# Kernel tuning notes

Hardware: AMD Instinct MI355X
Metric: run time of the kernel (lower is better)

Reference implementation:

```python
import jax, jax.numpy as jnp
import numpy as np

NUM_HEAD = 8
HEAD_DIM = 64
LMK = 32          # num_landmarks
WIN = 128         # window_size
DIM = 512         # transformer_dim == num_head*head_dim
EXT = WIN // 2    # ext_len in get_tiles_v2
TILE = 2 * EXT + WIN  # 256
SCALE = 1.0 / np.sqrt(HEAD_DIM)
NEG_INF = float('-inf')


def layernorm(x, g, b, eps=1e-5):
    m = jnp.mean(x, axis=-1, keepdims=True)
    v = jnp.mean((x - m) ** 2, axis=-1, keepdims=True)
    return (x - m) * jax.lax.rsqrt(v + eps) * g + b


def split_heads(x):
    b, s, _ = x.shape
    return x.reshape(b, s, NUM_HEAD, HEAD_DIM).transpose(0, 2, 1, 3)


def setup_inputs() -> dict:
    key = jax.random.key(0)
    ks = jax.random.split(key, 8)
    B, S = 2, 8192
    w = lambda k, sh: (jax.random.normal(k, sh, jnp.float32) * 0.02)
    return {
        'X': jax.random.normal(ks[0], (B, S, DIM), jnp.float32),
        'mask': jnp.ones((B, S), jnp.bool_),
        'Wq_w': w(ks[1], (DIM, DIM)), 'Wq_b': jnp.zeros((DIM,), jnp.float32),
        'Wk_w': w(ks[2], (DIM, DIM)), 'Wk_b': jnp.zeros((DIM,), jnp.float32),
        'Wv_w': w(ks[3], (DIM, DIM)), 'Wv_b': jnp.zeros((DIM,), jnp.float32),
        'Wo_w': w(ks[4], (DIM, DIM)), 'Wo_b': jnp.zeros((DIM,), jnp.float32),
        'ln_l_g': jnp.ones((DIM,), jnp.float32), 'ln_l_b': jnp.zeros((DIM,), jnp.float32),
        'ln_s_g': jnp.ones((DIM,), jnp.float32), 'ln_s_b': jnp.zeros((DIM,), jnp.float32),
        'dconv_w': w(ks[5], (DIM, NUM_HEAD * LMK)), 'dconv_b': jnp.zeros((NUM_HEAD * LMK,), jnp.float32),
    }


def reference(X, mask, Wq_w, Wq_b, Wk_w, Wk_b, Wv_w, Wv_b, Wo_w, Wo_b,
              ln_l_g, ln_l_b, ln_s_g, ln_s_b, dconv_w, dconv_b):
    B, S, D = X.shape
    G = S // WIN  # number of window groups
    pad_mask = ~mask  # True where padded

    Q = split_heads(X @ Wq_w + Wq_b) * SCALE                       # [B,H,S,dh]
    K = split_heads(layernorm(X @ Wk_w + Wk_b, ln_l_g, ln_l_b))    # [B,H,S,dh]
    V = split_heads(layernorm(X @ Wv_w + Wv_b, ln_l_g, ln_l_b))    # [B,H,S,dh]

    # --- landmark (long-range) compression ---
    hs = X @ dconv_w + dconv_b                                     # [B,S,H*L]
    hs = jnp.where(pad_mask[:, :, None], NEG_INF, hs)
    hs = jax.nn.softmax(hs.astype(jnp.float32), axis=1).astype(X.dtype)
    hs = hs.reshape(B, S, NUM_HEAD, LMK).transpose(0, 2, 3, 1)     # [B,H,L,S]
    K_c = jnp.einsum('bhls,bhsd->bhld', hs, K)                     # [B,H,L,dh]
    V_c = jnp.einsum('bhls,bhsd->bhld', hs, V)
    # dual LayerNorm on compressed keys/values (over combined head dim)
    K_c = split_heads(layernorm(K_c.transpose(0, 2, 1, 3).reshape(B, LMK, D), ln_s_g, ln_s_b))
    V_c = split_heads(layernorm(V_c.transpose(0, 2, 1, 3).reshape(B, LMK, D), ln_s_g, ln_s_b))

    attn_compress = jnp.einsum('bhsd,bhld->bhsl', Q, K_c)          # [B,H,S,L]

    # --- sliding-window (short-range) scores, v2 tiling ---
    idx = jnp.arange(G)[:, None] * WIN + jnp.arange(TILE)[None, :]  # [G,TILE] indices into padded seq
    K_pad = jnp.pad(K, ((0, 0), (0, 0), (EXT, EXT), (0, 0)))
    K_tiles = K_pad[:, :, idx, :]                                   # [B,H,G,TILE,dh]
    mask_pad = jnp.pad(pad_mask, ((0, 0), (EXT, EXT)), constant_values=True)
    mask_tiles = mask_pad[:, idx]                                   # [B,G,TILE]
    Q_tiles = Q.reshape(B, NUM_HEAD, G, WIN, HEAD_DIM)
    win = jnp.einsum('bhgwd,bhgtd->bhgwt', Q_tiles, K_tiles)
    win = jnp.where(mask_tiles[:, None, :, None, :], NEG_INF, win)
    win = win.reshape(B, NUM_HEAD, S, TILE)

    # --- joint softmax over [landmarks | window] ---
    all_scores = jnp.concatenate([attn_compress, win], axis=-1)     # [B,H,S,L+TILE]
    probs = jax.nn.softmax(all_scores.astype(jnp.float32), axis=-1).astype(X.dtype)
    probs = jnp.where(pad_mask[:, None, :, None], 0.0, probs)

    C = jnp.einsum('bhsl,bhld->bhsd', probs[..., :LMK], V_c)        # landmark contribution
    win_p = probs[..., LMK:].reshape(B, NUM_HEAD, G, WIN, TILE)
    V_pad = jnp.pad(V, ((0, 0), (0, 0), (EXT, EXT), (0, 0)))
    V_tiles = V_pad[:, :, idx, :]                                   # [B,H,G,TILE,dh]
    C = C + jnp.einsum('bhgwt,bhgtd->bhgwd', win_p, V_tiles).reshape(B, NUM_HEAD, S, HEAD_DIM)

    out = C.transpose(0, 2, 1, 3).reshape(B, S, D) @ Wo_w + Wo_b
    return out
```

## Files before the change

kernel.cpp:

```cpp
#include <hip/hip_runtime.h>

typedef unsigned short u16;
typedef unsigned int u32;
typedef __attribute__((ext_vector_type(8))) short bf16x8;
typedef __attribute__((ext_vector_type(4))) float f32x4;

#define DEVI static __device__ __forceinline__

DEVI float bf2f(u16 u){ u32 x = ((u32)u) << 16; float f; __builtin_memcpy(&f, &x, 4); return f; }
DEVI u16 f2bf(float f){ u32 x; __builtin_memcpy(&x, &f, 4); u32 r = x + 0x7FFFu + ((x >> 16) & 1u); return (u16)(r >> 16); }
DEVI u32 pk2(float a, float b){ return ((u32)f2bf(b) << 16) | (u32)f2bf(a); }

DEVI f32x4 mfma16(bf16x8 a, bf16x8 b, f32x4 c){
  return __builtin_amdgcn_mfma_f32_16x16x32_bf16(a, b, c, 0, 0, 0);
}

typedef __attribute__((address_space(3))) u32* lds_ptr_t;
typedef const __attribute__((address_space(1))) u32* gbl_ptr_t;
DEVI void gload16(const void* g, const void* l){
  __builtin_amdgcn_global_load_lds((gbl_ptr_t)(unsigned long long)g,
                                   (lds_ptr_t)(unsigned long long)l,
                                   16, 0, 0);
}

__global__ void cvt_x_kernel(const float* __restrict__ X, u16* __restrict__ Xb){
  int i = blockIdx.x * 256 + threadIdx.x;
  const f32x4* p = (const f32x4*)X;
  f32x4 a = p[(size_t)i*2], c = p[(size_t)i*2 + 1];
  bf16x8 v;
  v[0]=(short)f2bf(a[0]); v[1]=(short)f2bf(a[1]); v[2]=(short)f2bf(a[2]); v[3]=(short)f2bf(a[3]);
  v[4]=(short)f2bf(c[0]); v[5]=(short)f2bf(c[1]); v[6]=(short)f2bf(c[2]); v[7]=(short)f2bf(c[3]);
  *(bf16x8*)(Xb + (size_t)i*8) = v;
}

__global__ void transpose_all(const float* __restrict__ Wq, const float* __restrict__ Wk,
                              const float* __restrict__ Wv, const float* __restrict__ Wd,
                              const float* __restrict__ Wo,
                              const float* __restrict__ Wqb, const float* __restrict__ Wkb,
                              const float* __restrict__ Wvb, const float* __restrict__ Wdb,
                              u16* __restrict__ WT, float* __restrict__ biasAll)
{
  int id = blockIdx.x;
  if (id >= 1152){
    int c = (id - 1152) * 256 + threadIdx.x;
    float v = (c < 512) ? Wqb[c] : (c < 1024) ? Wkb[c-512] : (c < 1536) ? Wvb[c-1024] : Wdb[c-1536];
    biasAll[c] = v;
    return;
  }
  const float* W; int RO, N, local;
  if      (id < 256){ W = Wq; RO = 0;    N = 512; local = id; }
  else if (id < 512){ W = Wk; RO = 512;  N = 512; local = id - 256; }
  else if (id < 768){ W = Wv; RO = 1024; N = 512; local = id - 512; }
  else if (id < 896){ W = Wd; RO = 1536; N = 256; local = id - 768; }
  else              { W = Wo; RO = 1792; N = 512; local = id - 896; }
  int ntiles = N >> 5;
  int n0 = (local & (ntiles - 1)) * 32, k0 = (local / ntiles) * 32;
  __shared__ float tile[32][33];
  int tx = threadIdx.x & 31, ty = threadIdx.x >> 5;
  #pragma unroll
  for (int i = 0; i < 32; i += 8)
    tile[ty + i][tx] = W[(size_t)(k0 + ty + i) * N + n0 + tx];
  __syncthreads();
  #pragma unroll
  for (int i = 0; i < 32; i += 8)
    WT[(size_t)(RO + n0 + ty + i) * 512 + k0 + tx] = f2bf(tile[tx][ty + i]);
}

template<int MODE>
__global__ __launch_bounds__(256, 2) void gemmP(
    const u16* __restrict__ Abase, const u16* __restrict__ WT, const float* __restrict__ biasAll,
    u16* __restrict__ Qb, u16* __restrict__ Kb, u16* __restrict__ Vb,
    float* __restrict__ hsf, float* __restrict__ cmx, float* __restrict__ csm,
    float* __restrict__ pstatV, float* __restrict__ Cf)
{
  __shared__ __align__(16) u16 smem[32768];
  const int t = threadIdx.x, lane = t & 63, w = t >> 6;
  const int wm = w >> 1, wn = w & 1;
  const int lrow = lane & 15, lk = lane >> 4;
  int by, bx;
  {
    int xcd = blockIdx.x & 7, c = blockIdx.x >> 3;
    if (MODE == 0){ by = xcd*16 + c/14;   bx = c % 14; }
    else          { by = xcd*16 + (c>>2); bx = c & 3; }
  }
  const int m0 = by*128, n0 = bx*128;
  const u16* Bb = (MODE == 0) ? WT : (WT + (size_t)1792*512);

  const int srow = w*32 + (lane >> 3);
  const int scol = ((lane & 7) ^ (lane >> 3)) * 8;
  const u16* sA = Abase + (size_t)(m0 + srow)*512 + scol;
  const u16* sB = Bb    + (size_t)(n0 + srow)*512 + scol;

  f32x4 acc[4][4];
  const f32x4 fz = {0.f,0.f,0.f,0.f};
  #pragma unroll
  for (int i = 0; i < 4; i++)
    #pragma unroll
    for (int j = 0; j < 4; j++) acc[i][j] = fz;

  auto stage = [&](int tt){
    int slot = tt & 1;
    #pragma unroll
    for (int i = 0; i < 4; i++){
      gload16(sA + tt*64 + (size_t)i*4096, smem + slot*8192 + (w*4 + i)*512);
      gload16(sB + tt*64 + (size_t)i*4096, smem + 16384 + slot*8192 + (w*4 + i)*512);
    }
  };

  stage(0);
  stage(1);

  const int swz = (lrow & 7);
  #pragma unroll
  for (int tt = 0; tt < 8; tt++){
    if (tt < 7) asm volatile("s_waitcnt vmcnt(8)" ::: "memory");
    else        asm volatile("s_waitcnt vmcnt(0)" ::: "memory");
    __builtin_amdgcn_s_barrier();
    const u16* aS = smem + (tt & 1)*8192;
    const u16* bS = smem + 16384 + (tt & 1)*8192;
    #pragma unroll
    for (int ks = 0; ks < 2; ks++){
      bf16x8 af[4], bfv[4];
      #pragma unroll
      for (int mi = 0; mi < 4; mi++){
        int r = wm*64 + mi*16 + lrow;
        af[mi] = *(const bf16x8*)(aS + (r*8 + ((ks*4 + lk) ^ swz))*8);
      }
      #pragma unroll
      for (int ni = 0; ni < 4; ni++){
        int r = wn*64 + ni*16 + lrow;
        bfv[ni] = *(const bf16x8*)(bS + (r*8 + ((ks*4 + lk) ^ swz))*8);
      }
      #pragma unroll
      for (int mi = 0; mi < 4; mi++)
        #pragma unroll
        for (int ni = 0; ni < 4; ni++)
          acc[mi][ni] = mfma16(bfv[ni], af[mi], acc[mi][ni]);
    }
    __builtin_amdgcn_s_barrier();
    if (tt + 2 < 8) stage(tt + 2);
  }

  if (MODE == 1){
    #pragma unroll
    for (int mi = 0; mi < 4; mi++){
      int grow = m0 + wm*64 + mi*16 + lrow;
      #pragma unroll
      for (int ni = 0; ni < 4; ni++){
        int gcol0 = n0 + wn*64 + ni*16 + lk*4;
        f32x4 bv4 = *(const f32x4*)(biasAll + gcol0);
        f32x4 vv;
        #pragma unroll
        for (int rr = 0; rr < 4; rr++) vv[rr] = acc[mi][ni][rr] + bv4[rr];
        *(f32x4*)(Cf + (size_t)grow*512 + gcol0) = vv;
      }
    }
    return;
  }

  if (bx < 12){
    const int sel = bx >> 2;
    u16* dst = (sel == 0) ? Qb : (sel == 1) ? Kb : Vb;
    const float scale = (sel == 0) ? 0.125f : 1.0f;
    f32x4 bv4s[4];
    #pragma unroll
    for (int ni = 0; ni < 4; ni++)
      bv4s[ni] = *(const f32x4*)(biasAll + n0 + wn*64 + ni*16 + lk*4);
    #pragma unroll
    for (int mi = 0; mi < 4; mi++){
      int grow = m0 + wm*64 + mi*16 + lrow;
      int b = grow >> 13, s = grow & 8191;
      #pragma unroll
      for (int ni = 0; ni < 4; ni++){
        int gcol0 = n0 + wn*64 + ni*16 + lk*4;
        int lcol0 = gcol0 & 511, hh = lcol0 >> 6, dd0 = lcol0 & 63;
        float v0 = (acc[mi][ni][0] + bv4s[ni][0]) * scale;
        float v1 = (acc[mi][ni][1] + bv4s[ni][1]) * scale;
        float v2 = (acc[mi][ni][2] + bv4s[ni][2]) * scale;
        float v3 = (acc[mi][ni][3] + bv4s[ni][3]) * scale;
        u32* p = (u32*)(dst + (((size_t)(b*8 + hh))*8192 + s)*64 + dd0);
        p[0] = pk2(v0, v1);
        p[1] = pk2(v2, v3);
      }
    }
    if (sel == 2){
      float* vst = (float*)smem;
      __syncthreads();
      #pragma unroll
      for (int mi = 0; mi < 4; mi++){
        float s = 0.f, q = 0.f;
        #pragma unroll
        for (int ni = 0; ni < 4; ni++)
          #pragma unroll
          for (int rr = 0; rr < 4; rr++){
            float v = acc[mi][ni][rr] + bv4s[ni][rr];
            s += v; q += v*v;
          }
        s += __shfl_xor(s, 16); q += __shfl_xor(q, 16);
        s += __shfl_xor(s, 32); q += __shfl_xor(q, 32);
        if (lk == 0){
          int rloc = wm*64 + mi*16 + lrow;
          vst[rloc*4 + wn*2]     = s;
          vst[rloc*4 + wn*2 + 1] = q;
        }
      }
      __syncthreads();
      if (t < 128){
        float s = vst[t*4+0] + vst[t*4+2];
        float q = vst[t*4+1] + vst[t*4+3];
        pstatV[(size_t)(m0 + t)*8 + (bx - 8)*2]     = s;
        pstatV[(size_t)(m0 + t)*8 + (bx - 8)*2 + 1] = q;
      }
    }
  } else {
    float* pm = (float*)smem;
    float* ps = pm + 256;
    __syncthreads();
    #pragma unroll
    for (int ni = 0; ni < 4; ni++){
      int gcol0 = n0 + wn*64 + ni*16 + lk*4;
      int c0 = gcol0 - 1536;
      f32x4 bv4 = *(const f32x4*)(biasAll + gcol0);
      float mx[4], sm[4];
      #pragma unroll
      for (int rr = 0; rr < 4; rr++){ mx[rr] = -1e30f; sm[rr] = 0.f; }
      #pragma unroll
      for (int mi = 0; mi < 4; mi++){
        int grow = m0 + wm*64 + mi*16 + lrow;
        f32x4 v;
        #pragma unroll
        for (int rr = 0; rr < 4; rr++){
          v[rr] = acc[mi][ni][rr] + bv4[rr];
          float nm = fmaxf(mx[rr], v[rr]);
          sm[rr] = sm[rr]*__expf(mx[rr] - nm) + __expf(v[rr] - nm);
          mx[rr] = nm;
        }
        *(f32x4*)(hsf + (size_t)grow*256 + c0) = v;
      }
      #pragma unroll
      for (int rr = 0; rr < 4; rr++){
        #pragma unroll
        for (int d2 = 1; d2 < 16; d2 <<= 1){
          float om = __shfl_xor(mx[rr], d2), os = __shfl_xor(sm[rr], d2);
          float nm = fmaxf(mx[rr], om);
          sm[rr] = sm[rr]*__expf(mx[rr] - nm) + os*__expf(om - nm);
          mx[rr] = nm;
        }
      }
      if (lrow == 0){
        int cl = wn*64 + ni*16 + lk*4;
        f32x4 m4 = {mx[0], mx[1], mx[2], mx[3]};
        f32x4 s4 = {sm[0], sm[1], sm[2], sm[3]};
        *(f32x4*)(pm + wm*128 + cl) = m4;
        *(f32x4*)(ps + wm*128 + cl) = s4;
      }
    }
    __syncthreads();
    if (t < 128){
      float ma = pm[t], mb = pm[128 + t];
      float nm = fmaxf(ma, mb);
      float s = ps[t]*__expf(ma - nm) + ps[128 + t]*__expf(mb - nm);
      int b = m0 >> 13, chunk = (m0 & 8191) >> 7;
      int c = (n0 - 1536) + t;
      cmx[((size_t)b*64 + chunk)*256 + c] = nm;
      csm[((size_t)b*64 + chunk)*256 + c] = s;
    }
  }
}

__global__ __launch_bounds__(256) void ln_k(u16* __restrict__ Kb,
    const float* __restrict__ gg, const float* __restrict__ bb)
{
  const int lane = threadIdx.x & 63, w = threadIdx.x >> 6;
  const int row = blockIdx.x * 4 + w;
  const int b = row >> 13, si = row & 8191;
  const int hh = lane >> 3, d = (lane & 7) * 8;
  u16* p = Kb + (((size_t)(b*8 + hh))*8192 + si)*64 + d;
  bf16x8 raw = *(const bf16x8*)p;
  float x[8];
  #pragma unroll
  for (int j = 0; j < 8; j++) x[j] = bf2f((u16)raw[j]);
  float s = 0.f, q = 0.f;
  #pragma unroll
  for (int j = 0; j < 8; j++){ s += x[j]; q += x[j]*x[j]; }
  #pragma unroll
  for (int d2 = 1; d2 < 64; d2 <<= 1){ s += __shfl_xor(s, d2); q += __shfl_xor(q, d2); }
  float mean = s * (1.f/512.f);
  float var  = q * (1.f/512.f) - mean*mean;
  float rstd = rsqrtf(var + 1e-5f);
  int c0 = lane * 8;
  bf16x8 o;
  #pragma unroll
  for (int j = 0; j < 8; j++)
    o[j] = (short)f2bf((x[j] - mean) * rstd * gg[c0+j] + bb[c0+j]);
  *(bf16x8*)p = o;
}

__global__ __launch_bounds__(256) void transpose_ln_v(const u16* __restrict__ Vb,
    const float* __restrict__ pstatV, const float* __restrict__ gg, const float* __restrict__ bb,
    u16* __restrict__ VbT)
{
  __shared__ u16 tile[64][72];
  const int st = blockIdx.x, bh = blockIdx.y;
  const int b = bh >> 3, h = bh & 7;
  const int t = threadIdx.x;
  {
    int row = t >> 2, cc = (t & 3) * 16;
    int grow = b*8192 + st*64 + row;
    f32x4 p0 = *(const f32x4*)(pstatV + (size_t)grow*8);
    f32x4 p1 = *(const f32x4*)(pstatV + (size_t)grow*8 + 4);
    float mean = (p0[0]+p0[2]+p1[0]+p1[2]) * (1.f/512.f);
    float msq  = (p0[1]+p0[3]+p1[1]+p1[3]) * (1.f/512.f);
    float rstd = rsqrtf(msq - mean*mean + 1e-5f);
    const u16* src = Vb + ((size_t)bh*8192 + st*64 + row)*64 + cc;
    bf16x8 v0 = *(const bf16x8*)src, v1 = *(const bf16x8*)(src + 8);
    #pragma unroll
    for (int j = 0; j < 8; j++){
      int c = h*64 + cc + j;
      tile[row][cc + j]     = f2bf((bf2f((u16)v0[j]) - mean)*rstd*gg[c] + bb[c]);
      int c2 = c + 8;
      tile[row][cc + 8 + j] = f2bf((bf2f((u16)v1[j]) - mean)*rstd*gg[c2] + bb[c2]);
    }
  }
  __syncthreads();
  {
    int d = t >> 2, sc4 = (t & 3) * 16;
    bf16x8 o0, o1;
    #pragma unroll
    for (int i = 0; i < 8; i++) o0[i] = (short)tile[sc4 + i][d];
    #pragma unroll
    for (int i = 0; i < 8; i++) o1[i] = (short)tile[sc4 + 8 + i][d];
    u16* dst = VbT + ((size_t)bh*64 + d)*8192 + st*64 + sc4;
    *(bf16x8*)dst       = o0;
    *(bf16x8*)(dst + 8) = o1;
  }
}

__global__ void smax_comb(const float* __restrict__ cmax, const float* __restrict__ csum,
                          float* __restrict__ gmax, float* __restrict__ gsum){
  int b = blockIdx.x, c = threadIdx.x;
  float m[4], s[4];
  #pragma unroll
  for (int u = 0; u < 4; u++){ m[u] = -1e30f; s[u] = 0.f; }
  for (int ch = 0; ch < 64; ch += 4){
    #pragma unroll
    for (int u = 0; u < 4; u++){
      float cm = cmax[((size_t)b*64 + ch + u)*256 + c];
      float cs = csum[((size_t)b*64 + ch + u)*256 + c];
      float nm = fmaxf(m[u], cm);
      s[u] = s[u]*__expf(m[u] - nm) + cs*__expf(cm - nm);
      m[u] = nm;
    }
  }
  #pragma unroll
  for (int u = 1; u < 4; u++){
    float nm = fmaxf(m[0], m[u]);
    s[0] = s[0]*__expf(m[0]-nm) + s[u]*__expf(m[u]-nm);
    m[0] = nm;
  }
  gmax[b*256 + c] = m[0]; gsum[b*256 + c] = s[0];
}

__global__ __launch_bounds__(256) void cmp2_kernel(const float* __restrict__ hsf,
    const float* __restrict__ gmax, const float* __restrict__ gsum,
    const u16* __restrict__ Kb, const u16* __restrict__ Vb,
    const float* __restrict__ pstatV, const float* __restrict__ gg, const float* __restrict__ bb,
    float* __restrict__ pK, float* __restrict__ pV)
{
  __shared__ __align__(16) u16 Pt[32*72];
  __shared__ __align__(16) u16 Kt[64*72];
  __shared__ __align__(16) u16 Vt[64*72];
  const int sch = blockIdx.x, bh = blockIdx.y;
  const int b = bh >> 3, h = bh & 7;
  const int t = threadIdx.x, lane = t & 63, w = t >> 6;
  const int lrow = lane & 15, lk = lane >> 4;
  const int sl = lane;
  float gm[8], gi[8];
  #pragma unroll
  for (int j = 0; j < 8; j++){
    int c = h*32 + w*8 + j;
    gm[j] = gmax[b*256 + c];
    gi[j] = 1.0f / gsum[b*256 + c];
  }
  float glv[16], blv[16];
  #pragma unroll
  for (int j = 0; j < 16; j++){
    int c = h*64 + w*16 + j;
    glv[j] = gg[c]; blv[j] = bb[c];
  }
  const f32x4 fz = {0.f,0.f,0.f,0.f};
  f32x4 aK[2], aV[2];
  aK[0]=fz; aK[1]=fz; aV[0]=fz; aV[1]=fz;

  for (int tile = 0; tile < 4; ++tile){
    int s0 = sch*256 + tile*64;
    int grow = b*8192 + s0 + sl;
    {
      const float* src = hsf + (size_t)grow*256 + h*32 + w*8;
      f32x4 x0 = *(const f32x4*)src, x1 = *(const f32x4*)(src + 4);
      #pragma unroll
      for (int j = 0; j < 4; j++){
        Pt[(w*8 + j)*72 + sl]     = f2bf(__expf(x0[j] - gm[j])   * gi[j]);
        Pt[(w*8 + 4 + j)*72 + sl] = f2bf(__expf(x1[j] - gm[4+j]) * gi[4+j]);
      }
    }
    {
      const u16* ks = Kb + ((size_t)bh*8192 + s0 + sl)*64 + w*16;
      bf16x8 k0 = *(const bf16x8*)ks, k1 = *(const bf16x8*)(ks + 8);
      #pragma unroll
      for (int j = 0; j < 8; j++){
        Kt[(w*16 + j)*72 + sl]     = (u16)k0[j];
        Kt[(w*16 + 8 + j)*72 + sl] = (u16)k1[j];
      }
    }
    {
      f32x4 p0 = *(const f32x4*)(pstatV + (size_t)grow*8);
      f32x4 p1 = *(const f32x4*)(pstatV + (size_t)grow*8 + 4);
      float mean = (p0[0]+p0[2]+p1[0]+p1[2]) * (1.f/512.f);
      float msq  = (p0[1]+p0[3]+p1[1]+p1[3]) * (1.f/512.f);
      float rstd = rsqrtf(msq - mean*mean + 1e-5f);
      const u16* vs = Vb + ((size_t)bh*8192 + s0 + sl)*64 + w*16;
      bf16x8 v0 = *(const bf16x8*)vs, v1 = *(const bf16x8*)(vs + 8);
      #pragma unroll
      for (int j = 0; j < 8; j++){
        Vt[(w*16 + j)*72 + sl]     = f2bf((bf2f((u16)v0[j]) - mean)*rstd*glv[j]   + blv[j]);
        Vt[(w*16 + 8 + j)*72 + sl] = f2bf((bf2f((u16)v1[j]) - mean)*rstd*glv[8+j] + blv[8+j]);
      }
    }
    __syncthreads();
    #pragma unroll
    for (int ks = 0; ks < 2; ks++){
      bf16x8 a0 = *(const bf16x8*)(Pt + (lrow)*72      + ks*32 + lk*8);
      bf16x8 a1 = *(const bf16x8*)(Pt + (16 + lrow)*72 + ks*32 + lk*8);
      bf16x8 bK = *(const bf16x8*)(Kt + (w*16 + lrow)*72 + ks*32 + lk*8);
      bf16x8 bV = *(const bf16x8*)(Vt + (w*16 + lrow)*72 + ks*32 + lk*8);
      aK[0] = mfma16(a0, bK, aK[0]);
      aK[1] = mfma16(a1, bK, aK[1]);
      aV[0] = mfma16(a0, bV, aV[0]);
      aV[1] = mfma16(a1, bV, aV[1]);
    }
    __syncthreads();
  }
  size_t base = ((size_t)bh*32 + sch)*2048;
  #pragma unroll
  for (int li = 0; li < 2; li++){
    #pragma unroll
    for (int r = 0; r < 4; r++){
      size_t o = base + (size_t)(li*16 + lk*4 + r)*64 + w*16 + lrow;
      pK[o] = aK[li][r];
      pV[o] = aV[li][r];
    }
  }
}

__global__ __launch_bounds__(256) void ln_c_kernel(const float* __restrict__ pK, const float* __restrict__ pV,
    const float* __restrict__ gg, const float* __restrict__ bb,
    u16* __restrict__ Kcb, u16* __restrict__ VcT)
{
  __shared__ float red[4][4];
  const int b = blockIdx.x >> 5, l = blockIdx.x & 31;
  const int t = threadIdx.x, lane = t & 63, w = t >> 6;
  float xk[2], xv[2];
  #pragma unroll
  for (int q2 = 0; q2 < 2; q2++){
    int c = t + q2*256;
    int hh = c >> 6, d = c & 63;
    float sk = 0.f, sv = 0.f;
    for (int ch = 0; ch < 32; ch++){
      size_t idx = (((size_t)(b*8 + hh)*32 + ch)*2048) + l*64 + d;
      sk += pK[idx]; sv += pV[idx];
    }
    xk[q2] = sk; xv[q2] = sv;
  }
  float s1 = xk[0]+xk[1], q1 = xk[0]*xk[0]+xk[1]*xk[1];
  float s2 = xv[0]+xv[1], q2s = xv[0]*xv[0]+xv[1]*xv[1];
  #pragma unroll
  for (int d2 = 1; d2 < 64; d2 <<= 1){
    s1 += __shfl_xor(s1, d2); q1 += __shfl_xor(q1, d2);
    s2 += __shfl_xor(s2, d2); q2s += __shfl_xor(q2s, d2);
  }
  if (lane == 0){ red[0][w]=s1; red[1][w]=q1; red[2][w]=s2; red[3][w]=q2s; }
  __syncthreads();
  s1 = red[0][0]+red[0][1]+red[0][2]+red[0][3];
  q1 = red[1][0]+red[1][1]+red[1][2]+red[1][3];
  s2 = red[2][0]+red[2][1]+red[2][2]+red[2][3];
  q2s = red[3][0]+red[3][1]+red[3][2]+red[3][3];
  float mk = s1*(1.f/512.f), vk = q1*(1.f/512.f) - mk*mk, rk = rsqrtf(vk + 1e-5f);
  float mv = s2*(1.f/512.f), vvv = q2s*(1.f/512.f) - mv*mv, rv = rsqrtf(vvv + 1e-5f);
  #pragma unroll
  for (int q2 = 0; q2 < 2; q2++){
    int c = t + q2*256;
    int hh = c >> 6, d = c & 63;
    Kcb[(((size_t)(b*8 + hh))*32 + l)*64 + d] = f2bf((xk[q2]-mk)*rk*gg[c] + bb[c]);
    VcT[(((size_t)(b*8 + hh))*64 + d)*32 + l] = f2bf((xv[q2]-mv)*rv*gg[c] + bb[c]);
  }
}

__global__ __launch_bounds__(512, 4) void attn2_kernel(
    const u16* __restrict__ Qb, const u16* __restrict__ Kb, const u16* __restrict__ Kcb,
    const u16* __restrict__ VbT, const u16* __restrict__ VcT, u16* __restrict__ Cb)
{
  __shared__ __align__(16) char smem[74752];
  u16* Vt = (u16*)(smem + 36864);
  u16* Pl = (u16*)smem;

  const int g = (blockIdx.x & 7) * 8 + (blockIdx.x >> 3);
  const int h = blockIdx.y, b = blockIdx.z;
  const int bh = b*8 + h;
  const int t = threadIdx.x, lane = t & 63, w = t >> 6;
  const int lrow = lane & 15, lk = lane >> 4;
  const int s0 = g*128 - 64;
  const bf16x8 bz = {0,0,0,0,0,0,0,0};
  const f32x4 fz = {0.f,0.f,0.f,0.f};

  #pragma unroll
  for (int it = 0; it < 5; it++){
    int idx = it*512 + t;
    if (idx < 2304){
      int row = idx >> 3, kc = idx & 7;
      bf16x8 v = bz;
      if (row < 256){
        int sk = s0 + row;
        if (sk >= 0 && sk < 8192) v = *(const bf16x8*)(Kb + ((size_t)bh*8192 + sk)*64 + kc*8);
      } else {
        v = *(const bf16x8*)(Kcb + ((size_t)bh*32 + (row - 256))*64 + kc*8);
      }
      int off = row*128 + kc*16; off ^= (row & 7) << 4;
      *(bf16x8*)(smem + off) = v;
    }
  }
  #pragma unroll
  for (int it = 0; it < 4; it++){
    int idx = it*512 + t;
    int d = idx >> 5, cc = idx & 31;
    int sk = s0 + cc*8;
    bf16x8 v = bz;
    if (sk >= 0 && sk < 8192) v = *(const bf16x8*)(VbT + ((size_t)bh*64 + d)*8192 + sk);
    *(bf16x8*)(Vt + d*296 + cc*8) = v;
  }
  if (t < 256){
    int d = t >> 2, cc = t & 3;
    bf16x8 v = *(const bf16x8*)(VcT + ((size_t)bh*64 + d)*32 + cc*8);
    *(bf16x8*)(Vt + d*296 + 256 + cc*8) = v;
  }
  bf16x8 qf[2];
  #pragma unroll
  for (int ks = 0; ks < 2; ks++)
    qf[ks] = *(const bf16x8*)(Qb + ((size_t)bh*8192 + g*128 + w*16 + lrow)*64 + ks*32 + lk*8);

  __syncthreads();

  f32x4 sc[18];
  #pragma unroll
  for (int j = 0; j < 18; j++) sc[j] = fz;
  __builtin_amdgcn_s_setprio(1);
  #pragma unroll
  for (int j = 0; j < 18; j++){
    int row = j*16 + lrow;
    #pragma unroll
    for (int ks = 0; ks < 2; ks++){
      int off = row*128 + ks*64 + lk*16; off ^= (row & 7) << 4;
      bf16x8 kf = *(const bf16x8*)(smem + off);
      sc[j] = mfma16(kf, qf[ks], sc[j]);
    }
  }
  __builtin_amdgcn_s_setprio(0);

  #pragma unroll
  for (int j = 0; j < 16; j++){
    int sb = s0 + j*16 + lk*4;
    if (sb < 0 || sb >= 8192){
      sc[j][0] = -1e30f; sc[j][1] = -1e30f; sc[j][2] = -1e30f; sc[j][3] = -1e30f;
    }
  }

  float m = -1e30f;
  #pragma unroll
  for (int j = 0; j < 18; j++)
    m = fmaxf(m, fmaxf(fmaxf(sc[j][0], sc[j][1]), fmaxf(sc[j][2], sc[j][3])));
  m = fmaxf(m, __shfl_xor(m, 16));
  m = fmaxf(m, __shfl_xor(m, 32));
  float ssum = 0.f;
  #pragma unroll
  for (int j = 0; j < 18; j++){
    #pragma unroll
    for (int r = 0; r < 4; r++){
      float e = __expf(sc[j][r] - m);
      sc[j][r] = e; ssum += e;
    }
  }
  ssum += __shfl_xor(ssum, 16);
  ssum += __shfl_xor(ssum, 32);
  float inv = 1.0f / ssum;

  f32x4 ao[4];
  #pragma unroll
  for (int nj = 0; nj < 4; nj++) ao[nj] = fz;
  const int prow = w*16 + lrow;

  #pragma unroll
  for (int c = 0; c < 3; c++){
    __syncthreads();
    #pragma unroll
    for (int jj = 0; jj < 6; jj++){
      int j = c*6 + jj;
      u32* dst = (u32*)(Pl + prow*104 + jj*16 + lk*4);
      dst[0] = pk2(sc[j][0], sc[j][1]);
      dst[1] = pk2(sc[j][2], sc[j][3]);
    }
    __syncthreads();
    __builtin_amdgcn_s_setprio(1);
    #pragma unroll
    for (int ksl = 0; ksl < 3; ksl++){
      bf16x8 pb = *(const bf16x8*)(Pl + prow*104 + ksl*32 + lk*8);
      #pragma unroll
      for (int nj = 0; nj < 4; nj++){
        bf16x8 av = *(const bf16x8*)(Vt + (nj*16 + lrow)*296 + c*96 + ksl*32 + lk*8);
        ao[nj] = mfma16(av, pb, ao[nj]);
      }
    }
    __builtin_amdgcn_s_setprio(0);
  }

  const int qglob = g*128 + w*16 + lrow;
  #pragma unroll
  for (int nj = 0; nj < 4; nj++){
    u32* dst = (u32*)(Cb + ((size_t)b*8192 + qglob)*512 + h*64 + nj*16 + lk*4);
    dst[0] = pk2(ao[nj][0]*inv, ao[nj][1]*inv);
    dst[1] = pk2(ao[nj][2]*inv, ao[nj][3]*inv);
  }
}

constexpr size_t OFF_XB   = 0;
constexpr size_t OFF_WT   = OFF_XB  + 16777216;
constexpr size_t OFF_QB   = OFF_WT  + 2359296;
constexpr size_t OFF_KB   = OFF_QB  + 16777216;
constexpr size_t OFF_VB   = OFF_KB  + 16777216;
constexpr size_t OFF_CB   = OFF_VB  + 16777216;
constexpr size_t OFF_VBT  = OFF_CB  + 16777216;
constexpr size_t OFF_HSF  = OFF_VBT + 16777216;
constexpr size_t OFF_CMX  = OFF_HSF + 16777216;
constexpr size_t OFF_CSM  = OFF_CMX + 131072;
constexpr size_t OFF_GMX  = OFF_CSM + 131072;
constexpr size_t OFF_GSM  = OFF_GMX + 2048;
constexpr size_t OFF_PK   = OFF_GSM + 2048;
constexpr size_t OFF_PV   = OFF_PK  + 4194304;
constexpr size_t OFF_KCB  = OFF_PV  + 4194304;
constexpr size_t OFF_VCT  = OFF_KCB + 65536;
constexpr size_t OFF_BIAS = OFF_VCT + 65536;
constexpr size_t OFF_PSV  = OFF_BIAS + 8192;

extern "C" void kernel_launch(void* const* d_in, const int* in_sizes, int n_in,
                              void* d_out, int out_size, void* d_ws, size_t ws_size,
                              hipStream_t stream)
{
  const float* X    = (const float*)d_in[0];
  const float* Wq   = (const float*)d_in[2];
  const float* Wqb  = (const float*)d_in[3];
  const float* Wk   = (const float*)d_in[4];
  const float* Wkb  = (const float*)d_in[5];
  const float* Wv   = (const float*)d_in[6];
  const float* Wvb  = (const float*)d_in[7];
  const float* Wo   = (const float*)d_in[8];
  const float* Wob  = (const float*)d_in[9];
  const float* lnlg = (const float*)d_in[10];
  const float* lnlb = (const float*)d_in[11];
  const float* lnsg = (const float*)d_in[12];
  const float* lnsb = (const float*)d_in[13];
  const float* Wd   = (const float*)d_in[14];
  const float* Wdb  = (const float*)d_in[15];
  float* out = (float*)d_out;

  char* ws = (char*)d_ws;
  u16*   Xb   = (u16*)(ws + OFF_XB);
  u16*   WT   = (u16*)(ws + OFF_WT);
  u16*   Qb   = (u16*)(ws + OFF_QB);
  u16*   Kb   = (u16*)(ws + OFF_KB);
  u16*   Vb   = (u16*)(ws + OFF_VB);
  u16*   Cbp  = (u16*)(ws + OFF_CB);
  u16*   VbT  = (u16*)(ws + OFF_VBT);
  float* hsf  = (float*)(ws + OFF_HSF);
  float* cmx  = (float*)(ws + OFF_CMX);
  float* csm  = (float*)(ws + OFF_CSM);
  float* gmx  = (float*)(ws + OFF_GMX);
  float* gsm  = (float*)(ws + OFF_GSM);
  float* pK   = (float*)(ws + OFF_PK);
  float* pV   = (float*)(ws + OFF_PV);
  u16*   Kcb  = (u16*)(ws + OFF_KCB);
  u16*   VcT  = (u16*)(ws + OFF_VCT);
  float* biasAll = (float*)(ws + OFF_BIAS);
  float* pstatV  = (float*)(ws + OFF_PSV);

  cvt_x_kernel<<<dim3(4096), dim3(256), 0, stream>>>(X, Xb);
  transpose_all<<<dim3(1159), dim3(256), 0, stream>>>(Wq, Wk, Wv, Wd, Wo,
                                                      Wqb, Wkb, Wvb, Wdb, WT, biasAll);

  gemmP<0><<<dim3(1792), dim3(256), 0, stream>>>(Xb, WT, biasAll, Qb, Kb, Vb,
                                                 hsf, cmx, csm, pstatV, nullptr);

  ln_k<<<dim3(4096), dim3(256), 0, stream>>>(Kb, lnlg, lnlb);
  transpose_ln_v<<<dim3(128,16), dim3(256), 0, stream>>>(Vb, pstatV, lnlg, lnlb, VbT);

  smax_comb<<<dim3(2), dim3(256), 0, stream>>>(cmx, csm, gmx, gsm);

  cmp2_kernel<<<dim3(32,16), dim3(256), 0, stream>>>(hsf, gmx, gsm, Kb, Vb, pstatV,
                                                     lnlg, lnlb, pK, pV);
  ln_c_kernel<<<dim3(64), dim3(256), 0, stream>>>(pK, pV, lnsg, lnsb, Kcb, VcT);

  attn2_kernel<<<dim3(64,8,2), dim3(512), 0, stream>>>(Qb, Kb, Kcb, VbT, VcT, Cbp);

  gemmP<1><<<dim3(512), dim3(256), 0, stream>>>(Cbp, WT, Wob, nullptr, nullptr, nullptr,
                                                nullptr, nullptr, nullptr, nullptr, out);
}
```

Before: 170.4 us.

## Persistent-loop projection GEMM and defer K layernorm to consumers via row stats

The projection GEMM now runs as a persistent grid of 512 blocks, each looping over output tiles, instead of launching 1792 blocks. The K layernorm no longer rewrites K in place. A stats-only kernel stores each row's mean and rstd, and the compression and attention kernels apply the normalization while loading K. This removes one full read-modify-write pass over K, at the cost of extra per-element arithmetic and stat loads inside the attention staging loop. The stored K values are also rounded differently, since raw bf16 is normalized on load.

```diff
diff --git a/kernel.cpp b/kernel.cpp
--- a/kernel.cpp
+++ b/kernel.cpp
@@ -4,6 +4,7 @@
 typedef unsigned int u32;
 typedef __attribute__((ext_vector_type(8))) short bf16x8;
 typedef __attribute__((ext_vector_type(4))) float f32x4;
+typedef __attribute__((ext_vector_type(2))) float f32x2;
 
 #define DEVI static __device__ __forceinline__
 
@@ -77,205 +78,209 @@
   const int t = threadIdx.x, lane = t & 63, w = t >> 6;
   const int wm = w >> 1, wn = w & 1;
   const int lrow = lane & 15, lk = lane >> 4;
-  int by, bx;
-  {
-    int xcd = blockIdx.x & 7, c = blockIdx.x >> 3;
-    if (MODE == 0){ by = xcd*16 + c/14;   bx = c % 14; }
-    else          { by = xcd*16 + (c>>2); bx = c & 3; }
-  }
-  const int m0 = by*128, n0 = bx*128;
-  const u16* Bb = (MODE == 0) ? WT : (WT + (size_t)1792*512);
-
+  const u16* Bbase = (MODE == 0) ? WT : (WT + (size_t)1792*512);
   const int srow = w*32 + (lane >> 3);
   const int scol = ((lane & 7) ^ (lane >> 3)) * 8;
-  const u16* sA = Abase + (size_t)(m0 + srow)*512 + scol;
-  const u16* sB = Bb    + (size_t)(n0 + srow)*512 + scol;
-
-  f32x4 acc[4][4];
+  const int swz = (lrow & 7);
+  const int NCH = (MODE == 0) ? 1792 : 512;
   const f32x4 fz = {0.f,0.f,0.f,0.f};
-  #pragma unroll
-  for (int i = 0; i < 4; i++)
-    #pragma unroll
-    for (int j = 0; j < 4; j++) acc[i][j] = fz;
-
-  auto stage = [&](int tt){
-    int slot = tt & 1;
-    #pragma unroll
-    for (int i = 0; i < 4; i++){
-      gload16(sA + tt*64 + (size_t)i*4096, smem + slot*8192 + (w*4 + i)*512);
-      gload16(sB + tt*64 + (size_t)i*4096, smem + 16384 + slot*8192 + (w*4 + i)*512);
-    }
-  };
-
-  stage(0);
-  stage(1);
-
-  const int swz = (lrow & 7);
-  #pragma unroll
-  for (int tt = 0; tt < 8; tt++){
-    if (tt < 7) asm volatile("s_waitcnt vmcnt(8)" ::: "memory");
-    else        asm volatile("s_waitcnt vmcnt(0)" ::: "memory");
-    __builtin_amdgcn_s_barrier();
-    const u16* aS = smem + (tt & 1)*8192;
-    const u16* bS = smem + 16384 + (tt & 1)*8192;
-    #pragma unroll
-    for (int ks = 0; ks < 2; ks++){
-      bf16x8 af[4], bfv[4];
+
+  for (int ch = blockIdx.x; ch < NCH; ch += 512){
+    int by, bx;
+    {
+      int xcd = ch & 7, c = ch >> 3;
+      if (MODE == 0){ by = xcd*16 + c/14;   bx = c % 14; }
+      else          { by = xcd*16 + (c>>2); bx = c & 3; }
+    }
+    const int m0 = by*128, n0 = bx*128;
+    const u16* sA = Abase + (size_t)(m0 + srow)*512 + scol;
+    const u16* sB = Bbase + (size_t)(n0 + srow)*512 + scol;
+
+    f32x4 acc[4][4];
+    #pragma unroll
+    for (int i = 0; i < 4; i++)
+      #pragma unroll
+      for (int j = 0; j < 4; j++) acc[i][j] = fz;
+
+    auto stage = [&](int tt){
+      int slot = tt & 1;
+      #pragma unroll
+      for (int i = 0; i < 4; i++){
+        gload16(sA + tt*64 + (size_t)i*4096, smem + slot*8192 + (w*4 + i)*512);
+        gload16(sB + tt*64 + (size_t)i*4096, smem + 16384 + slot*8192 + (w*4 + i)*512);
+      }
+    };
+
+    stage(0);
+    stage(1);
+
+    #pragma unroll
+    for (int tt = 0; tt < 8; tt++){
+      if (tt < 7) asm volatile("s_waitcnt vmcnt(8)" ::: "memory");
+      else        asm volatile("s_waitcnt vmcnt(0)" ::: "memory");
+      __builtin_amdgcn_s_barrier();
+      const u16* aS = smem + (tt & 1)*8192;
+      const u16* bS = smem + 16384 + (tt & 1)*8192;
+      #pragma unroll
+      for (int ks = 0; ks < 2; ks++){
+        bf16x8 af[4], bfv[4];
+        #pragma unroll
+        for (int mi = 0; mi < 4; mi++){
+          int r = wm*64 + mi*16 + lrow;
+          af[mi] = *(const bf16x8*)(aS + (r*8 + ((ks*4 + lk) ^ swz))*8);
+        }
+        #pragma unroll
+        for (int ni = 0; ni < 4; ni++){
+          int r = wn*64 + ni*16 + lrow;
+          bfv[ni] = *(const bf16x8*)(bS + (r*8 + ((ks*4 + lk) ^ swz))*8);
+        }
+        #pragma unroll
+        for (int mi = 0; mi < 4; mi++)
+          #pragma unroll
+          for (int ni = 0; ni < 4; ni++)
+            acc[mi][ni] = mfma16(bfv[ni], af[mi], acc[mi][ni]);
+      }
+      __builtin_amdgcn_s_barrier();
+      if (tt + 2 < 8) stage(tt + 2);
+    }
+
+    if (MODE == 1){
       #pragma unroll
       for (int mi = 0; mi < 4; mi++){
-        int r = wm*64 + mi*16 + lrow;
-        af[mi] = *(const bf16x8*)(aS + (r*8 + ((ks*4 + lk) ^ swz))*8);
-      }
-      #pragma unroll
-      for (int ni = 0; ni < 4; ni++){
-        int r = wn*64 + ni*16 + lrow;
-        bfv[ni] = *(const bf16x8*)(bS + (r*8 + ((ks*4 + lk) ^ swz))*8);
-      }
-      #pragma unroll
-      for (int mi = 0; mi < 4; mi++)
-        #pragma unroll
-        for (int ni = 0; ni < 4; ni++)
-          acc[mi][ni] = mfma16(bfv[ni], af[mi], acc[mi][ni]);
-    }
-    __builtin_amdgcn_s_barrier();
-    if (tt + 2 < 8) stage(tt + 2);
-  }
-
-  if (MODE == 1){
-    #pragma unroll
-    for (int mi = 0; mi < 4; mi++){
-      int grow = m0 + wm*64 + mi*16 + lrow;
+        int grow = m0 + wm*64 + mi*16 + lrow;
+        #pragma unroll
+        for (int ni = 0; ni < 4; ni++){
+          int gcol0 = n0 + wn*64 + ni*16 + lk*4;
+          f32x4 bv4 = *(const f32x4*)(biasAll + gcol0);
+          f32x4 vv;
+          #pragma unroll
+          for (int rr = 0; rr < 4; rr++) vv[rr] = acc[mi][ni][rr] + bv4[rr];
+          *(f32x4*)(Cf + (size_t)grow*512 + gcol0) = vv;
+        }
+      }
+      continue;
+    }
+
+    if (bx < 12){
+      const int sel = bx >> 2;
+      u16* dst = (sel == 0) ? Qb : (sel == 1) ? Kb : Vb;
+      const float scale = (sel == 0) ? 0.125f : 1.0f;
+      f32x4 bv4s[4];
+      #pragma unroll
+      for (int ni = 0; ni < 4; ni++)
+        bv4s[ni] = *(const f32x4*)(biasAll + n0 + wn*64 + ni*16 + lk*4);
+      #pragma unroll
+      for (int mi = 0; mi < 4; mi++){
+        int grow = m0 + wm*64 + mi*16 + lrow;
+        int b = grow >> 13, s = grow & 8191;
+        #pragma unroll
+        for (int ni = 0; ni < 4; ni++){
+          int gcol0 = n0 + wn*64 + ni*16 + lk*4;
+          int lcol0 = gcol0 & 511, hh = lcol0 >> 6, dd0 = lcol0 & 63;
+          float v0 = (acc[mi][ni][0] + bv4s[ni][0]) * scale;
+          float v1 = (acc[mi][ni][1] + bv4s[ni][1]) * scale;
+          float v2 = (acc[mi][ni][2] + bv4s[ni][2]) * scale;
+          float v3 = (acc[mi][ni][3] + bv4s[ni][3]) * scale;
+          u32* p = (u32*)(dst + (((size_t)(b*8 + hh))*8192 + s)*64 + dd0);
+          p[0] = pk2(v0, v1);
+          p[1] = pk2(v2, v3);
+        }
+      }
+      if (sel == 2){
+        float* vst = (float*)smem;
+        __syncthreads();
+        #pragma unroll
+        for (int mi = 0; mi < 4; mi++){
+          float s = 0.f, q = 0.f;
+          #pragma unroll
+          for (int ni = 0; ni < 4; ni++)
+            #pragma unroll
+            for (int rr = 0; rr < 4; rr++){
+              float v = acc[mi][ni][rr] + bv4s[ni][rr];
+              s += v; q += v*v;
+            }
+          s += __shfl_xor(s, 16); q += __shfl_xor(q, 16);
+          s += __shfl_xor(s, 32); q += __shfl_xor(q, 32);
+          if (lk == 0){
+            int rloc = wm*64 + mi*16 + lrow;
+            vst[rloc*4 + wn*2]     = s;
+            vst[rloc*4 + wn*2 + 1] = q;
+          }
+        }
+        __syncthreads();
+        if (t < 128){
+          float s = vst[t*4+0] + vst[t*4+2];
+          float q = vst[t*4+1] + vst[t*4+3];
+          pstatV[(size_t)(m0 + t)*8 + (bx - 8)*2]     = s;
+          pstatV[(size_t)(m0 + t)*8 + (bx - 8)*2 + 1] = q;
+        }
+      }
+    } else {
+      float* pm = (float*)smem;
+      float* ps = pm + 256;
+      __syncthreads();
       #pragma unroll
       for (int ni = 0; ni < 4; ni++){
         int gcol0 = n0 + wn*64 + ni*16 + lk*4;
+        int c0 = gcol0 - 1536;
         f32x4 bv4 = *(const f32x4*)(biasAll + gcol0);
-        f32x4 vv;
-        #pragma unroll
-        for (int rr = 0; rr < 4; rr++) vv[rr] = acc[mi][ni][rr] + bv4[rr];
-        *(f32x4*)(Cf + (size_t)grow*512 + gcol0) = vv;
-      }
-    }
-    return;
-  }
-
-  if (bx < 12){
-    const int sel = bx >> 2;
-    u16* dst = (sel == 0) ? Qb : (sel == 1) ? Kb : Vb;
-    const float scale = (sel == 0) ? 0.125f : 1.0f;
-    f32x4 bv4s[4];
-    #pragma unroll
-    for (int ni = 0; ni < 4; ni++)
-      bv4s[ni] = *(const f32x4*)(biasAll + n0 + wn*64 + ni*16 + lk*4);
-    #pragma unroll
-    for (int mi = 0; mi < 4; mi++){
-      int grow = m0 + wm*64 + mi*16 + lrow;
-      int b = grow >> 13, s = grow & 8191;
-      #pragma unroll
-      for (int ni = 0; ni < 4; ni++){
-        int gcol0 = n0 + wn*64 + ni*16 + lk*4;
-        int lcol0 = gcol0 & 511, hh = lcol0 >> 6, dd0 = lcol0 & 63;
-        float v0 = (acc[mi][ni][0] + bv4s[ni][0]) * scale;
-        float v1 = (acc[mi][ni][1] + bv4s[ni][1]) * scale;
-        float v2 = (acc[mi][ni][2] + bv4s[ni][2]) * scale;
-        float v3 = (acc[mi][ni][3] + bv4s[ni][3]) * scale;
-        u32* p = (u32*)(dst + (((size_t)(b*8 + hh))*8192 + s)*64 + dd0);
-        p[0] = pk2(v0, v1);
-        p[1] = pk2(v2, v3);
-      }
-    }
-    if (sel == 2){
-      float* vst = (float*)smem;
-      __syncthreads();
-      #pragma unroll
-      for (int mi = 0; mi < 4; mi++){
-        float s = 0.f, q = 0.f;
-        #pragma unroll
-        for (int ni = 0; ni < 4; ni++)
+        float mx[4], sm[4];
+        #pragma unroll
+        for (int rr = 0; rr < 4; rr++){ mx[rr] = -1e30f; sm[rr] = 0.f; }
+        #pragma unroll
+        for (int mi = 0; mi < 4; mi++){
+          int grow = m0 + wm*64 + mi*16 + lrow;
+          f32x4 v;
           #pragma unroll
           for (int rr = 0; rr < 4; rr++){
-            float v = acc[mi][ni][rr] + bv4s[ni][rr];
-            s += v; q += v*v;
+            v[rr] = acc[mi][ni][rr] + bv4[rr];
+            float nm = fmaxf(mx[rr], v[rr]);
+            sm[rr] = sm[rr]*__expf(mx[rr] - nm) + __expf(v[rr] - nm);
+            mx[rr] = nm;
           }
-        s += __shfl_xor(s, 16); q += __shfl_xor(q, 16);
-        s += __shfl_xor(s, 32); q += __shfl_xor(q, 32);
-        if (lk == 0){
-          int rloc = wm*64 + mi*16 + lrow;
-          vst[rloc*4 + wn*2]     = s;
-          vst[rloc*4 + wn*2 + 1] = q;
+          *(f32x4*)(hsf + (size_t)grow*256 + c0) = v;
+        }
+        #pragma unroll
+        for (int rr = 0; rr < 4; rr++){
+          #pragma unroll
+          for (int d2 = 1; d2 < 16; d2 <<= 1){
+            float om = __shfl_xor(mx[rr], d2), os = __shfl_xor(sm[rr], d2);
+            float nm = fmaxf(mx[rr], om);
+            sm[rr] = sm[rr]*__expf(mx[rr] - nm) + os*__expf(om - nm);
+            mx[rr] = nm;
+          }
+        }
+        if (lrow == 0){
+          int cl = wn*64 + ni*16 + lk*4;
+          f32x4 m4 = {mx[0], mx[1], mx[2], mx[3]};
+          f32x4 s4 = {sm[0], sm[1], sm[2], sm[3]};
+          *(f32x4*)(pm + wm*128 + cl) = m4;
+          *(f32x4*)(ps + wm*128 + cl) = s4;
         }
       }
       __syncthreads();
       if (t < 128){
-        float s = vst[t*4+0] + vst[t*4+2];
-        float q = vst[t*4+1] + vst[t*4+3];
-        pstatV[(size_t)(m0 + t)*8 + (bx - 8)*2]     = s;
-        pstatV[(size_t)(m0 + t)*8 + (bx - 8)*2 + 1] = q;
-      }
-    }
-  } else {
-    float* pm = (float*)smem;
-    float* ps = pm + 256;
+        float ma = pm[t], mb = pm[128 + t];
+        float nm = fmaxf(ma, mb);
+        float s = ps[t]*__expf(ma - nm) + ps[128 + t]*__expf(mb - nm);
+        int b = m0 >> 13, chunk = (m0 & 8191) >> 7;
+        int c = (n0 - 1536) + t;
+        cmx[((size_t)b*64 + chunk)*256 + c] = nm;
+        csm[((size_t)b*64 + chunk)*256 + c] = s;
+      }
+    }
     __syncthreads();
-    #pragma unroll
-    for (int ni = 0; ni < 4; ni++){
-      int gcol0 = n0 + wn*64 + ni*16 + lk*4;
-      int c0 = gcol0 - 1536;
-      f32x4 bv4 = *(const f32x4*)(biasAll + gcol0);
-      float mx[4], sm[4];
-      #pragma unroll
-      for (int rr = 0; rr < 4; rr++){ mx[rr] = -1e30f; sm[rr] = 0.f; }
-      #pragma unroll
-      for (int mi = 0; mi < 4; mi++){
-        int grow = m0 + wm*64 + mi*16 + lrow;
-        f32x4 v;
-        #pragma unroll
-        for (int rr = 0; rr < 4; rr++){
-          v[rr] = acc[mi][ni][rr] + bv4[rr];
-          float nm = fmaxf(mx[rr], v[rr]);
-          sm[rr] = sm[rr]*__expf(mx[rr] - nm) + __expf(v[rr] - nm);
-          mx[rr] = nm;
-        }
-        *(f32x4*)(hsf + (size_t)grow*256 + c0) = v;
-      }
-      #pragma unroll
-      for (int rr = 0; rr < 4; rr++){
-        #pragma unroll
-        for (int d2 = 1; d2 < 16; d2 <<= 1){
-          float om = __shfl_xor(mx[rr], d2), os = __shfl_xor(sm[rr], d2);
-          float nm = fmaxf(mx[rr], om);
-          sm[rr] = sm[rr]*__expf(mx[rr] - nm) + os*__expf(om - nm);
-          mx[rr] = nm;
-        }
-      }
-      if (lrow == 0){
-        int cl = wn*64 + ni*16 + lk*4;
-        f32x4 m4 = {mx[0], mx[1], mx[2], mx[3]};
-        f32x4 s4 = {sm[0], sm[1], sm[2], sm[3]};
-        *(f32x4*)(pm + wm*128 + cl) = m4;
-        *(f32x4*)(ps + wm*128 + cl) = s4;
-      }
-    }
-    __syncthreads();
-    if (t < 128){
-      float ma = pm[t], mb = pm[128 + t];
-      float nm = fmaxf(ma, mb);
-      float s = ps[t]*__expf(ma - nm) + ps[128 + t]*__expf(mb - nm);
-      int b = m0 >> 13, chunk = (m0 & 8191) >> 7;
-      int c = (n0 - 1536) + t;
-      cmx[((size_t)b*64 + chunk)*256 + c] = nm;
-      csm[((size_t)b*64 + chunk)*256 + c] = s;
-    }
-  }
-}
-
-__global__ __launch_bounds__(256) void ln_k(u16* __restrict__ Kb,
-    const float* __restrict__ gg, const float* __restrict__ bb)
+  }
+}
+
+__global__ __launch_bounds__(256) void ln_stats_k(const u16* __restrict__ Kb,
+    float* __restrict__ kstat)
 {
   const int lane = threadIdx.x & 63, w = threadIdx.x >> 6;
   const int row = blockIdx.x * 4 + w;
   const int b = row >> 13, si = row & 8191;
   const int hh = lane >> 3, d = (lane & 7) * 8;
-  u16* p = Kb + (((size_t)(b*8 + hh))*8192 + si)*64 + d;
+  const u16* p = Kb + (((size_t)(b*8 + hh))*8192 + si)*64 + d;
   bf16x8 raw = *(const bf16x8*)p;
   float x[8];
   #pragma unroll
@@ -288,12 +293,10 @@
   float mean = s * (1.f/512.f);
   float var  = q * (1.f/512.f) - mean*mean;
   float rstd = rsqrtf(var + 1e-5f);
-  int c0 = lane * 8;
-  bf16x8 o;
-  #pragma unroll
-  for (int j = 0; j < 8; j++)
-    o[j] = (short)f2bf((x[j] - mean) * rstd * gg[c0+j] + bb[c0+j]);
-  *(bf16x8*)p = o;
+  if (lane == 0){
+    kstat[(size_t)row*2]     = mean;
+    kstat[(size_t)row*2 + 1] = rstd;
+  }
 }
 
 __global__ __launch_bounds__(256) void transpose_ln_v(const u16* __restrict__ Vb,
@@ -364,7 +367,8 @@
 __global__ __launch_bounds__(256) void cmp2_kernel(const float* __restrict__ hsf,
     const float* __restrict__ gmax, const float* __restrict__ gsum,
     const u16* __restrict__ Kb, const u16* __restrict__ Vb,
-    const float* __restrict__ pstatV, const float* __restrict__ gg, const float* __restrict__ bb,
+    const float* __restrict__ kstat, const float* __restrict__ pstatV,
+    const float* __restrict__ gg, const float* __restrict__ bb,
     float* __restrict__ pK, float* __restrict__ pV)
 {
   __shared__ __align__(16) u16 Pt[32*72];
@@ -405,12 +409,13 @@
       }
     }
     {
+      f32x2 st = *(const f32x2*)(kstat + (size_t)grow*2);
       const u16* ks = Kb + ((size_t)bh*8192 + s0 + sl)*64 + w*16;
       bf16x8 k0 = *(const bf16x8*)ks, k1 = *(const bf16x8*)(ks + 8);
       #pragma unroll
       for (int j = 0; j < 8; j++){
-        Kt[(w*16 + j)*72 + sl]     = (u16)k0[j];
-        Kt[(w*16 + 8 + j)*72 + sl] = (u16)k1[j];
+        Kt[(w*16 + j)*72 + sl]     = f2bf((bf2f((u16)k0[j]) - st[0])*st[1]*glv[j]   + blv[j]);
+        Kt[(w*16 + 8 + j)*72 + sl] = f2bf((bf2f((u16)k1[j]) - st[0])*st[1]*glv[8+j] + blv[8+j]);
       }
     }
     {
@@ -498,7 +503,9 @@
 
 __global__ __launch_bounds__(512, 4) void attn2_kernel(
     const u16* __restrict__ Qb, const u16* __restrict__ Kb, const u16* __restrict__ Kcb,
-    const u16* __restrict__ VbT, const u16* __restrict__ VcT, u16* __restrict__ Cb)
+    const u16* __restrict__ VbT, const u16* __restrict__ VcT,
+    const float* __restrict__ kstat, const float* __restrict__ lnlg, const float* __restrict__ lnlb,
+    u16* __restrict__ Cb)
 {
   __shared__ __align__(16) char smem[74752];
   u16* Vt = (u16*)(smem + 36864);
@@ -513,6 +520,16 @@
   const bf16x8 bz = {0,0,0,0,0,0,0,0};
   const f32x4 fz = {0.f,0.f,0.f,0.f};
 
+  float g8[8], b8[8];
+  {
+    int kcl = t & 7;
+    #pragma unroll
+    for (int j = 0; j < 8; j++){
+      int c = h*64 + kcl*8 + j;
+      g8[j] = lnlg[c]; b8[j] = lnlb[c];
+    }
+  }
+
   #pragma unroll
   for (int it = 0; it < 5; it++){
     int idx = it*512 + t;
@@ -521,7 +538,13 @@
       bf16x8 v = bz;
       if (row < 256){
         int sk = s0 + row;
-        if (sk >= 0 && sk < 8192) v = *(const bf16x8*)(Kb + ((size_t)bh*8192 + sk)*64 + kc*8);
+        if (sk >= 0 && sk < 8192){
+          v = *(const bf16x8*)(Kb + ((size_t)bh*8192 + sk)*64 + kc*8);
+          f32x2 st = *(const f32x2*)(kstat + (size_t)(b*8192 + sk)*2);
+          #pragma unroll
+          for (int j = 0; j < 8; j++)
+            v[j] = (short)f2bf((bf2f((u16)v[j]) - st[0])*st[1]*g8[j] + b8[j]);
+        }
       } else {
         v = *(const bf16x8*)(Kcb + ((size_t)bh*32 + (row - 256))*64 + kc*8);
       }
@@ -649,6 +672,7 @@
 constexpr size_t OFF_VCT  = OFF_KCB + 65536;
 constexpr size_t OFF_BIAS = OFF_VCT + 65536;
 constexpr size_t OFF_PSV  = OFF_BIAS + 8192;
+constexpr size_t OFF_KST  = OFF_PSV + 524288;
 
 extern "C" void kernel_launch(void* const* d_in, const int* in_sizes, int n_in,
                               void* d_out, int out_size, void* d_ws, size_t ws_size,
@@ -690,24 +714,26 @@
   u16*   VcT  = (u16*)(ws + OFF_VCT);
   float* biasAll = (float*)(ws + OFF_BIAS);
   float* pstatV  = (float*)(ws + OFF_PSV);
+  float* kstat   = (float*)(ws + OFF_KST);
 
   cvt_x_kernel<<<dim3(4096), dim3(256), 0, stream>>>(X, Xb);
   transpose_all<<<dim3(1159), dim3(256), 0, stream>>>(Wq, Wk, Wv, Wd, Wo,
                                                       Wqb, Wkb, Wvb, Wdb, WT, biasAll);
 
-  gemmP<0><<<dim3(1792), dim3(256), 0, stream>>>(Xb, WT, biasAll, Qb, Kb, Vb,
-                                                 hsf, cmx, csm, pstatV, nullptr);
-
-  ln_k<<<dim3(4096), dim3(256), 0, stream>>>(Kb, lnlg, lnlb);
+  gemmP<0><<<dim3(512), dim3(256), 0, stream>>>(Xb, WT, biasAll, Qb, Kb, Vb,
+                                                hsf, cmx, csm, pstatV, nullptr);
+
+  ln_stats_k<<<dim3(4096), dim3(256), 0, stream>>>(Kb, kstat);
   transpose_ln_v<<<dim3(128,16), dim3(256), 0, stream>>>(Vb, pstatV, lnlg, lnlb, VbT);
 
   smax_comb<<<dim3(2), dim3(256), 0, stream>>>(cmx, csm, gmx, gsm);
 
-  cmp2_kernel<<<dim3(32,16), dim3(256), 0, stream>>>(hsf, gmx, gsm, Kb, Vb, pstatV,
+  cmp2_kernel<<<dim3(32,16), dim3(256), 0, stream>>>(hsf, gmx, gsm, Kb, Vb, kstat, pstatV,
                                                      lnlg, lnlb, pK, pV);
   ln_c_kernel<<<dim3(64), dim3(256), 0, stream>>>(pK, pV, lnsg, lnsb, Kcb, VcT);
 
-  attn2_kernel<<<dim3(64,8,2), dim3(512), 0, stream>>>(Qb, Kb, Kcb, VbT, VcT, Cbp);
+  attn2_kernel<<<dim3(64,8,2), dim3(512), 0, stream>>>(Qb, Kb, Kcb, VbT, VcT,
+                                                       kstat, lnlg, lnlb, Cbp);
 
   gemmP<1><<<dim3(512), dim3(256), 0, stream>>>(Cbp, WT, Wob, nullptr, nullptr, nullptr,
                                                 nullptr, nullptr, nullptr, nullptr, out);
```

After: 171.0 us. About the same (+0.3%).
